# Kernel tuning notes

Hardware: AMD Instinct MI355X
Metric: run time of the kernel (lower is better)

Reference implementation:

```python
import jax, jax.numpy as jnp
import numpy as np

D_IN = 1024
D_OUT = 1024
NUM_HEADS = 16
HEAD_DIM = D_OUT // NUM_HEADS


def setup_inputs() -> dict:
    key = jax.random.key(0)
    ks = jax.random.split(key, 6)
    s = 0.02
    return {
        "x": jax.random.normal(ks[0], (4, 2048, D_IN), dtype=jnp.float32),
        "Wq": jax.random.normal(ks[1], (D_IN, D_OUT), dtype=jnp.float32) * s,
        "Wk": jax.random.normal(ks[2], (D_IN, D_OUT), dtype=jnp.float32) * s,
        "Wv": jax.random.normal(ks[3], (D_IN, D_OUT), dtype=jnp.float32) * s,
        "Wo": jax.random.normal(ks[4], (D_OUT, D_OUT), dtype=jnp.float32) * s,
        "bo": jax.random.normal(ks[5], (D_OUT,), dtype=jnp.float32) * s,
    }


def reference(x, Wq, Wk, Wv, Wo, bo):
    B, T, _ = x.shape
    H, Dh = NUM_HEADS, HEAD_DIM
    # projections -> [B, H, T, Dh]
    q = (x @ Wq).reshape(B, T, H, Dh).transpose(0, 2, 1, 3)
    k = (x @ Wk).reshape(B, T, H, Dh).transpose(0, 2, 1, 3)
    v = (x @ Wv).reshape(B, T, H, Dh).transpose(0, 2, 1, 3)
    # scores [B, H, T, T]
    scores = jnp.einsum('bhqd,bhkd->bhqk', q, k)
    causal = jnp.triu(jnp.ones((T, T), dtype=bool), k=1)
    scores = jnp.where(causal, -jnp.inf, scores)
    attn = jax.nn.softmax(scores / jnp.sqrt(jnp.float32(Dh)), axis=-1)
    # dropout=0.0 -> identity
    ctx = jnp.einsum('bhqk,bhkd->bhqd', attn, v)
    ctx = ctx.transpose(0, 2, 1, 3).reshape(B, T, H * Dh)
    return ctx @ Wo + bo
```

## Files before the change

kernel.cpp:

```cpp
#include <hip/hip_runtime.h>
#include <hip/hip_bf16.h>
#include <stdint.h>

#define TSEQ 2048
#define DMODEL 1024

typedef __attribute__((ext_vector_type(8))) short bf16x8;
typedef __attribute__((ext_vector_type(4))) float f32x4;
typedef __attribute__((ext_vector_type(16))) float f32x16;
typedef __attribute__((ext_vector_type(2))) int int2v;

union Frag { bf16x8 v; uint4 q; };

__device__ __forceinline__ uint16_t f2bfu(float f) {
  uint32_t u = __builtin_bit_cast(uint32_t, f);
  u += 0x7fffu + ((u >> 16) & 1u);
  return (uint16_t)(u >> 16);
}

__device__ __forceinline__ uint32_t pk2bf(float a, float b) {
  return ((uint32_t)f2bfu(b) << 16) | f2bfu(a);
}

__device__ __forceinline__ uint32_t cvtpk(float a, float b) {
  uint32_t r;
  asm("v_cvt_pk_bf16_f32 %0, %1, %2" : "=v"(r) : "v"(a), "v"(b));
  return r;
}

__device__ __forceinline__ void plane32swap(uint32_t& a, uint32_t& b) {
#if __has_builtin(__builtin_amdgcn_permlane32_swap)
  int2v r = __builtin_amdgcn_permlane32_swap((int)a, (int)b, false, false);
  a = (uint32_t)r[0];
  b = (uint32_t)r[1];
#else
  const uint32_t sa = (uint32_t)__shfl_xor((int)a, 32);
  const uint32_t sb = (uint32_t)__shfl_xor((int)b, 32);
  const bool hi = (threadIdx.x & 63) >= 32;
  const uint32_t na = hi ? sb : a;
  const uint32_t nb = hi ? b : sa;
  a = na;
  b = nb;
#endif
}

__device__ __forceinline__ float fexp2(float x) {
#if __has_builtin(__builtin_amdgcn_exp2f)
  return __builtin_amdgcn_exp2f(x);
#else
  return exp2f(x);
#endif
}

__device__ __forceinline__ void gload_lds16(const void* g, void* l) {
  __builtin_amdgcn_global_load_lds(
      (const __attribute__((address_space(1))) void*)g,
      (__attribute__((address_space(3))) void*)l, 16, 0, 0);
}


__global__ __launch_bounds__(256) void cvt_x_kernel(const float* __restrict__ x,
                                                    uint16_t* __restrict__ xb, int n4) {
  int i = blockIdx.x * 256 + threadIdx.x;
  if (i >= n4) return;
  float4 v = ((const float4*)x)[i];
  ushort4 o;
  o.x = f2bfu(v.x); o.y = f2bfu(v.y); o.z = f2bfu(v.z); o.w = f2bfu(v.w);
  ((ushort4*)xb)[i] = o;
}

__global__ __launch_bounds__(256) void cvt_w_kernel(const float* __restrict__ Wq,
    const float* __restrict__ Wk, const float* __restrict__ Wv, const float* __restrict__ Wo,
    uint16_t* __restrict__ Wqkvt, uint16_t* __restrict__ Wot) {
  const float* src = (blockIdx.z == 0) ? Wq : (blockIdx.z == 1) ? Wk
                   : (blockIdx.z == 2) ? Wv : Wo;
  uint16_t* dst = (blockIdx.z < 3) ? (Wqkvt + (size_t)blockIdx.z * DMODEL * DMODEL) : Wot;
  const float wscale = (blockIdx.z == 0) ? 0.125f * 1.4426950408889634f : 1.0f;
  __shared__ float tile[32][33];
  const int x0 = blockIdx.x * 32, y0 = blockIdx.y * 32;
  for (int ii = 0; ii < 4; ii++) {
    int i = threadIdx.y + ii * 8;
    tile[i][threadIdx.x] = src[(size_t)(y0 + i) * DMODEL + x0 + threadIdx.x];
  }
  __syncthreads();
  for (int ii = 0; ii < 4; ii++) {
    int i = threadIdx.y + ii * 8;
    dst[(size_t)(x0 + i) * DMODEL + y0 + threadIdx.x] = f2bfu(tile[threadIdx.x][i] * wscale);
  }
}

__device__ __forceinline__ void stage256(const char* Gb, int kb, char* ldsT, int tid) {
#pragma unroll
  for (int r = 0; r < 4; ++r) {
    const int u = tid + r * 512;
    const int row = u >> 3;
    const int sc = ((u & 7) * 16) ^ ((row & 7) << 4);
    gload_lds16(Gb + (size_t)row * 2048 + kb + sc, ldsT + u * 16);
  }
}


__device__ __forceinline__ void gemm256sq_core(const char* Ab, const char* Bb,
                                               char* lds,
                                               f32x4 (&acc)[8][4]) {
  const int tid = threadIdx.x;
  const int lane = tid & 63;
  const int w = tid >> 6;
  const int lr = lane & 15, lg = lane >> 4;
  const int wmb = (w >> 2) * 128;
  const int wnb = (w & 3) * 64;
  char* const A0 = lds;
  char* const A1 = lds + 32768;
  char* const B0 = lds + 65536;
  char* const B1 = lds + 98304;

#pragma unroll
  for (int i = 0; i < 8; i++)
#pragma unroll
    for (int j = 0; j < 4; j++) acc[i][j] = (f32x4){0.f, 0.f, 0.f, 0.f};

  stage256(Ab, 0, A0, tid);
  stage256(Bb, 0, B0, tid);
  for (int t = 0; t < 16; ++t) {
    const char* At = (t & 1) ? A1 : A0;
    const char* Bt = (t & 1) ? B1 : B0;
    char* nA = (t & 1) ? A0 : A1;
    char* nB = (t & 1) ? B0 : B1;
    if (t + 1 < 16) {
      stage256(Ab, (t + 1) * 128, nA, tid);
      asm volatile("s_waitcnt vmcnt(4)" ::: "memory");
    } else {
      asm volatile("s_waitcnt vmcnt(0)" ::: "memory");
    }
    __builtin_amdgcn_s_barrier();
    __builtin_amdgcn_sched_barrier(0);

    Frag bf0[4], bf1[4];
#pragma unroll
    for (int ni = 0; ni < 4; ni++) {
      const int row = wnb + ni * 16 + lr;
      const int swz = (row & 7) << 4;
      bf0[ni].q = *(const uint4*)(Bt + row * 128 + ((lg * 16) ^ swz));
      bf1[ni].q = *(const uint4*)(Bt + row * 128 + ((64 + lg * 16) ^ swz));
    }
#pragma unroll
    for (int ph = 0; ph < 4; ph++) {
      Frag a0[2], a1[2];
#pragma unroll
      for (int i = 0; i < 2; i++) {
        const int row = wmb + (2 * ph + i) * 16 + lr;
        const int swz = (row & 7) << 4;
        a0[i].q = *(const uint4*)(At + row * 128 + ((lg * 16) ^ swz));
        a1[i].q = *(const uint4*)(At + row * 128 + ((64 + lg * 16) ^ swz));
      }
      __builtin_amdgcn_s_setprio(1);
#pragma unroll
      for (int i = 0; i < 2; i++) {
        const int mi = 2 * ph + i;
#pragma unroll
        for (int ni = 0; ni < 4; ni++) {
          acc[mi][ni] = __builtin_amdgcn_mfma_f32_16x16x32_bf16(a0[i].v, bf0[ni].v,
                                                                acc[mi][ni], 0, 0, 0);
          acc[mi][ni] = __builtin_amdgcn_mfma_f32_16x16x32_bf16(a1[i].v, bf1[ni].v,
                                                                acc[mi][ni], 0, 0, 0);
        }
      }
      __builtin_amdgcn_s_setprio(0);
      if (ph == 0 && t + 1 < 16) stage256(Bb, (t + 1) * 128, nB, tid);
    }
    __builtin_amdgcn_s_barrier();
  }
}


__device__ __forceinline__ void g8_stage_p1(const char* Ab, int kb, char* ldsA, int tid) {
#pragma unroll
  for (int r = 0; r < 3; ++r) {
    const int u = tid + r * 512;
    const int row = u >> 3;
    const int sc = ((u & 7) * 16) ^ ((row & 7) << 4);
    gload_lds16(Ab + (size_t)row * 2048 + kb + sc, ldsA + u * 16);
  }
}

__device__ __forceinline__ void g8_stage_p2(const char* Ab, const char* Bb, int kb,
                                            char* ldsA, char* ldsB, int tid) {
  {
    const int u = tid + 3 * 512;
    const int row = u >> 3;
    const int sc = ((u & 7) * 16) ^ ((row & 7) << 4);
    gload_lds16(Ab + (size_t)row * 2048 + kb + sc, ldsA + u * 16);
  }
#pragma unroll
  for (int r = 0; r < 2; ++r) {
    const int u = tid + r * 512;
    const int row = u >> 3;
    const int sc = ((u & 7) * 16) ^ ((row & 7) << 4);
    gload_lds16(Bb + (size_t)row * 2048 + kb + sc, ldsB + u * 16);
  }
}

__device__ __forceinline__ void gemm256x128_core(const char* Ab, const char* Bb,
                                                 char* lds,
                                                 f32x4 (&acc)[4][4]) {
  const int tid = threadIdx.x;
  const int lane = tid & 63;
  const int w = tid >> 6;
  const int lr = lane & 15, lg = lane >> 4;
  const int wmb = (w >> 1) * 64;
  const int wnb = (w & 1) * 64;
  char* const A0 = lds;
  char* const A1 = lds + 32768;
  char* const B0 = lds + 65536;
  char* const B1 = lds + 81920;

#pragma unroll
  for (int i = 0; i < 4; i++)
#pragma unroll
    for (int j = 0; j < 4; j++) acc[i][j] = (f32x4){0.f, 0.f, 0.f, 0.f};

  g8_stage_p1(Ab, 0, A0, tid);
  g8_stage_p2(Ab, Bb, 0, A0, B0, tid);
  for (int t = 0; t < 16; ++t) {
    const char* At = (t & 1) ? A1 : A0;
    const char* Bt = (t & 1) ? B1 : B0;
    char* nA = (t & 1) ? A0 : A1;
    char* nB = (t & 1) ? B0 : B1;
    if (t + 1 < 16) {
      g8_stage_p1(Ab, (t + 1) * 128, nA, tid);
      asm volatile("s_waitcnt vmcnt(3)" ::: "memory");
    } else {
      asm volatile("s_waitcnt vmcnt(0)" ::: "memory");
    }
    __builtin_amdgcn_s_barrier();
    __builtin_amdgcn_sched_barrier(0);

    Frag bf0[4], bf1[4];
#pragma unroll
    for (int ni = 0; ni < 4; ni++) {
      const int row = wnb + ni * 16 + lr;
      const int swz = (row & 7) << 4;
      bf0[ni].q = *(const uint4*)(Bt + row * 128 + ((lg * 16) ^ swz));
      bf1[ni].q = *(const uint4*)(Bt + row * 128 + ((64 + lg * 16) ^ swz));
    }
    Frag pa0[2], pa1[2];
#pragma unroll
    for (int mi = 0; mi < 2; mi++) {
      const int row = wmb + mi * 16 + lr;
      const int swz = (row & 7) << 4;
      pa0[mi].q = *(const uint4*)(At + row * 128 + ((lg * 16) ^ swz));
      pa1[mi].q = *(const uint4*)(At + row * 128 + ((64 + lg * 16) ^ swz));
    }
    __builtin_amdgcn_s_setprio(1);
#pragma unroll
    for (int mi = 0; mi < 2; mi++)
#pragma unroll
      for (int ni = 0; ni < 4; ni++) {
        acc[mi][ni] = __builtin_amdgcn_mfma_f32_16x16x32_bf16(pa0[mi].v, bf0[ni].v,
                                                              acc[mi][ni], 0, 0, 0);
        acc[mi][ni] = __builtin_amdgcn_mfma_f32_16x16x32_bf16(pa1[mi].v, bf1[ni].v,
                                                              acc[mi][ni], 0, 0, 0);
      }
    __builtin_amdgcn_s_setprio(0);

    if (t + 1 < 16) g8_stage_p2(Ab, Bb, (t + 1) * 128, nA, nB, tid);
#pragma unroll
    for (int mi = 2; mi < 4; mi++) {
      const int row = wmb + mi * 16 + lr;
      const int swz = (row & 7) << 4;
      Frag qa0, qa1;
      qa0.q = *(const uint4*)(At + row * 128 + ((lg * 16) ^ swz));
      qa1.q = *(const uint4*)(At + row * 128 + ((64 + lg * 16) ^ swz));
      __builtin_amdgcn_s_setprio(1);
#pragma unroll
      for (int ni = 0; ni < 4; ni++) {
        acc[mi][ni] = __builtin_amdgcn_mfma_f32_16x16x32_bf16(qa0.v, bf0[ni].v,
                                                              acc[mi][ni], 0, 0, 0);
        acc[mi][ni] = __builtin_amdgcn_mfma_f32_16x16x32_bf16(qa1.v, bf1[ni].v,
                                                              acc[mi][ni], 0, 0, 0);
      }
      __builtin_amdgcn_s_setprio(0);
    }
    __builtin_amdgcn_s_barrier();
  }
}


__global__ __launch_bounds__(512, 2) void gemm_qkv_fused(const uint16_t* __restrict__ Xb,
    const uint16_t* __restrict__ Wt, uint16_t* __restrict__ Qo,
    uint16_t* __restrict__ Ko, uint16_t* __restrict__ Vt) {
  __shared__ __align__(16) char lds[131072];
  const int tid = threadIdx.x, w = tid >> 6, lane = tid & 63;
  const int lr = lane & 15, lg = lane >> 4;

  if (blockIdx.x < 256) {
    const int m0 = (blockIdx.x & 31) * 256;
    const int n0 = (blockIdx.x >> 5) * 256;
    f32x4 acc[8][4];
    gemm256sq_core((const char*)Xb + (size_t)m0 * 2048, (const char*)Wt + (size_t)n0 * 2048,
                   lds, acc);
    const int wmb = (w >> 2) * 128, wnb = (w & 3) * 64;
#pragma unroll
    for (int mi = 0; mi < 8; mi++)
#pragma unroll
      for (int ni = 0; ni < 4; ni++) {
        const int col = n0 + wnb + ni * 16 + lr;
        const int p = col >> 10, c = col & 1023, h = c >> 6, d = c & 63;
#pragma unroll
        for (int r = 0; r < 4; r++) {
          const int row = m0 + wmb + mi * 16 + 4 * lg + r;
          const int bb = row >> 11, t = row & 2047;
          const int bh = bb * 16 + h;
          const uint16_t val = f2bfu(acc[mi][ni][r]);
          if (p == 0) Qo[((size_t)bh * TSEQ + t) * 64 + d] = val;
          else        Ko[((size_t)bh * TSEQ + t) * 64 + d] = val;
        }
      }
  } else {
    const int vb = blockIdx.x - 256;
    const int m0 = (vb & 31) * 256;
    const int n0 = (vb >> 5) * 128;
    const uint16_t* Wtv = Wt + (size_t)2048 * 1024;
    f32x4 acc[4][4];
    gemm256x128_core((const char*)Xb + (size_t)m0 * 2048, (const char*)Wtv + (size_t)n0 * 2048,
                     lds, acc);
    const int wmb = (w >> 1) * 64;
    char* vr = lds + (w & 1) * 33792;
#pragma unroll
    for (int mi = 0; mi < 4; mi++)
#pragma unroll
      for (int ni = 0; ni < 4; ni++) {
        const int d = ni * 16 + lr;
        const int tl = wmb + mi * 16 + 4 * lg;
        uint2 pr;
        pr.x = cvtpk(acc[mi][ni][0], acc[mi][ni][1]);
        pr.y = cvtpk(acc[mi][ni][2], acc[mi][ni][3]);
        *(uint2*)(vr + d * 528 + tl * 2) = pr;
      }
    __syncthreads();
    const int bb = m0 >> 11, t0 = m0 & 2047;
    const int h0 = n0 >> 6;
#pragma unroll
    for (int j = 0; j < 8; j++) {
      const int linear = (tid + j * 512) * 16;
      const int rg = linear >> 15;
      const int rem = linear & 32767;
      const int d = rem >> 9;
      const int toff = rem & 511;
      const uint4 val = *(const uint4*)(lds + rg * 33792 + d * 528 + toff);
      const int bh = bb * 16 + h0 + rg;
      *(uint4*)((char*)Vt + ((size_t)(bh * 64 + d) * TSEQ + t0) * 2 + toff) = val;
    }
  }
}


__device__ __forceinline__ void stage_kv(const char* Kb, const char* Vb, int kv0,
                                         char* kdst, char* vdst, int tid) {
  const int w1024 = (tid >> 6) * 1024;
#pragma unroll
  for (int i = 0; i < 2; i++) {
    const int o = i * 4096 + tid * 16;
    const int row = o >> 7;
    const int scol = (o & 127) ^ ((row & 7) << 4);
    gload_lds16(Kb + (size_t)(kv0 + row) * 128 + scol, kdst + i * 4096 + w1024);
    gload_lds16(Vb + (size_t)row * 4096 + kv0 * 2 + scol, vdst + i * 4096 + w1024);
  }
}

__global__ __launch_bounds__(256, 4) void attn_kernel(const uint16_t* __restrict__ Qw,
    const uint16_t* __restrict__ Kw, const uint16_t* __restrict__ Vtw,
    uint16_t* __restrict__ Ctx) {
  const int bid = blockIdx.x;
  const int c = bid & 255;
  const int rd = bid >> 8;
  const int g = c >> 6;
  int qt;
  if (rd == 0)      qt = 15 - g;
  else if (rd == 1) qt = 8 + g;
  else if (rd == 2) qt = 7 - g;
  else              qt = g;
  const int bh = c & 63;
  const int tid = threadIdx.x;
  const int w = tid >> 6, lane = tid & 63;
  const int lq = lane & 31;
  const int hi = lane >> 5;
  const int wq0 = qt * 128 + w * 32;

  const char* Qb = (const char*)Qw + (size_t)bh * TSEQ * 128;
  const char* Kb = (const char*)Kw + (size_t)bh * TSEQ * 128;
  const char* Vb = (const char*)Vtw + (size_t)bh * 64 * 4096;

  __shared__ __align__(16) char kbuf[2][8192];
  __shared__ __align__(16) char vbuf[2][8192];

  Frag qa[4];
#pragma unroll
  for (int kc = 0; kc < 4; kc++)
    qa[kc].q = *(const uint4*)(Qb + (size_t)(wq0 + lq) * 128 + kc * 32 + hi * 16);

  f32x16 o0 = 0.f, o1 = 0.f;
  float mrun = -1e30f, lrun = 0.f;

  const int nt = 2 * qt + 2;
  stage_kv(Kb, Vb, 0, kbuf[0], vbuf[0], tid);
  int cur = 0;
  for (int t = 0; t < nt; ++t) {
    const int kv0 = t * 64;
    if (t + 1 < nt) {
      stage_kv(Kb, Vb, kv0 + 64, kbuf[cur ^ 1], vbuf[cur ^ 1], tid);
      asm volatile("s_waitcnt vmcnt(4)" ::: "memory");
    } else {
      asm volatile("s_waitcnt vmcnt(0)" ::: "memory");
    }
    __builtin_amdgcn_s_barrier();
    __builtin_amdgcn_sched_barrier(0);

    if (kv0 <= wq0 + 31) {
      const char* Kt = kbuf[cur];
      const char* Vt = vbuf[cur];
      f32x16 s[2];
#pragma unroll
      for (int kvh = 0; kvh < 2; kvh++) {
        f32x16 acc = 0.f;
#pragma unroll
        for (int kc = 0; kc < 4; kc++) {
          const int row = kvh * 32 + lq;
          Frag kf;
          kf.q = *(const uint4*)(Kt + row * 128 + ((kc * 32 + hi * 16) ^ ((row & 7) << 4)));
          acc = __builtin_amdgcn_mfma_f32_32x32x16_bf16(kf.v, qa[kc].v, acc, 0, 0, 0);
        }
        s[kvh] = acc;
      }
      if (kv0 + 63 > wq0) {
        const int q_abs = wq0 + lq;
#pragma unroll
        for (int kvh = 0; kvh < 2; kvh++)
#pragma unroll
          for (int r = 0; r < 16; r++) {
            const int kv_abs = kv0 + kvh * 32 + (r & 3) + 8 * (r >> 2) + 4 * hi;
            if (kv_abs > q_abs) s[kvh][r] = -1e30f;
          }
      }
      float t8[8];
#pragma unroll
      for (int i = 0; i < 8; i++)
        t8[i] = fmaxf(fmaxf(s[0][2 * i], s[0][2 * i + 1]),
                      fmaxf(s[1][2 * i], s[1][2 * i + 1]));
      float t4a = fmaxf(t8[0], t8[1]), t4b = fmaxf(t8[2], t8[3]);
      float t4c = fmaxf(t8[4], t8[5]), t4d = fmaxf(t8[6], t8[7]);
      float mt = fmaxf(fmaxf(t4a, t4b), fmaxf(t4c, t4d));
      mt = fmaxf(mt, __shfl_xor(mt, 32));
      if (!__all(mt - mrun <= 8.0f)) {
        const float mnew = fmaxf(mrun, mt);
        const float corr = fexp2(mrun - mnew);
        mrun = mnew;
        lrun *= corr;
        o0 *= corr;
        o1 *= corr;
      }
#pragma unroll
      for (int kvh = 0; kvh < 2; kvh++)
#pragma unroll
        for (int r = 0; r < 16; r++) s[kvh][r] = fexp2(s[kvh][r] - mrun);
      float ps = 0.f;
#pragma unroll
      for (int kvh = 0; kvh < 2; kvh++)
#pragma unroll
        for (int r = 0; r < 16; r++) ps += s[kvh][r];
      ps += __shfl_xor(ps, 32);
      lrun += ps;
      uint32_t pk[2][8];
#pragma unroll
      for (int kvh = 0; kvh < 2; kvh++)
#pragma unroll
        for (int j = 0; j < 8; j++)
          pk[kvh][j] = cvtpk(s[kvh][2 * j], s[kvh][2 * j + 1]);
#pragma unroll
      for (int c16 = 0; c16 < 4; c16++) {
        const int kvh = c16 >> 1, cl = c16 & 1;
        uint32_t x0 = pk[kvh][4 * cl + 0], y0 = pk[kvh][4 * cl + 2];
        uint32_t x1 = pk[kvh][4 * cl + 1], y1 = pk[kvh][4 * cl + 3];
        plane32swap(x0, y0);
        plane32swap(x1, y1);
        Frag pb;
        pb.q.x = x0;
        pb.q.y = x1;
        pb.q.z = y0;
        pb.q.w = y1;
#pragma unroll
        for (int dblk = 0; dblk < 2; dblk++) {
          const int row = dblk * 32 + lq;
          Frag vf;
          vf.q = *(const uint4*)(Vt + row * 128 + ((c16 * 32 + hi * 16) ^ ((row & 7) << 4)));
          if (dblk == 0)
            o0 = __builtin_amdgcn_mfma_f32_32x32x16_bf16(vf.v, pb.v, o0, 0, 0, 0);
          else
            o1 = __builtin_amdgcn_mfma_f32_32x32x16_bf16(vf.v, pb.v, o1, 0, 0, 0);
        }
      }
    }
    __builtin_amdgcn_s_barrier();
    cur ^= 1;
  }

  const int bb = bh >> 4, hh = bh & 15;
  const float inv = 1.0f / lrun;
  const int q_abs = wq0 + lq;
  uint16_t* crow = Ctx + ((size_t)bb * TSEQ + q_abs) * DMODEL + hh * 64;
#pragma unroll
  for (int dblk = 0; dblk < 2; dblk++)
#pragma unroll
    for (int g2 = 0; g2 < 4; g2++) {
      const float a0 = (dblk ? o1[4 * g2 + 0] : o0[4 * g2 + 0]) * inv;
      const float a1 = (dblk ? o1[4 * g2 + 1] : o0[4 * g2 + 1]) * inv;
      const float a2 = (dblk ? o1[4 * g2 + 2] : o0[4 * g2 + 2]) * inv;
      const float a3 = (dblk ? o1[4 * g2 + 3] : o0[4 * g2 + 3]) * inv;
      uint2 st;
      st.x = cvtpk(a0, a1);
      st.y = cvtpk(a2, a3);
      *(uint2*)(crow + dblk * 32 + 8 * g2 + 4 * hi) = st;
    }
}


__global__ __launch_bounds__(512, 2) void gemm_out_kernel(const uint16_t* __restrict__ Cb,
    const uint16_t* __restrict__ Wot, const float* __restrict__ bo,
    float* __restrict__ out) {
  __shared__ __align__(16) char lds[98304];
  const int m0 = (blockIdx.x & 31) * 256;
  const int n0 = (blockIdx.x >> 5) * 128;
  f32x4 acc[4][4];
  gemm256x128_core((const char*)Cb + (size_t)m0 * 2048, (const char*)Wot + (size_t)n0 * 2048,
                   lds, acc);

  const int tid = threadIdx.x, w = tid >> 6, lane = tid & 63;
  const int lr = lane & 15, lg = lane >> 4;
  const int wmb = (w >> 1) * 64, wnb = (w & 1) * 64;
#pragma unroll
  for (int mi = 0; mi < 4; mi++)
#pragma unroll
    for (int ni = 0; ni < 4; ni++) {
      const int col = n0 + wnb + ni * 16 + lr;
      const float bias = bo[col];
#pragma unroll
      for (int r = 0; r < 4; r++) {
        const int row = m0 + wmb + mi * 16 + 4 * lg + r;
        out[(size_t)row * DMODEL + col] = acc[mi][ni][r] + bias;
      }
    }
}


extern "C" void kernel_launch(void* const* d_in, const int* in_sizes, int n_in,
                              void* d_out, int out_size, void* d_ws, size_t ws_size,
                              hipStream_t stream) {
  const float* x  = (const float*)d_in[0];
  const float* Wq = (const float*)d_in[1];
  const float* Wk = (const float*)d_in[2];
  const float* Wv = (const float*)d_in[3];
  const float* Wo = (const float*)d_in[4];
  const float* bo = (const float*)d_in[5];
  float* out = (float*)d_out;

  char* ws = (char*)d_ws;
  uint16_t* Xb    = (uint16_t*)(ws);
  uint16_t* Ctx   = (uint16_t*)(ws);
  uint16_t* Wqkvt = (uint16_t*)(ws + (16u << 20));
  uint16_t* Wot   = (uint16_t*)(ws + (22u << 20));
  uint16_t* Qw    = (uint16_t*)(ws + (24u << 20));
  uint16_t* Kw    = (uint16_t*)(ws + (40u << 20));
  uint16_t* Vtw   = (uint16_t*)(ws + (56u << 20));
  (void)ws_size; (void)in_sizes; (void)n_in; (void)out_size;

  cvt_x_kernel<<<8192, 256, 0, stream>>>(x, Xb, 2097152);
  cvt_w_kernel<<<dim3(32, 32, 4), dim3(32, 8), 0, stream>>>(Wq, Wk, Wv, Wo, Wqkvt, Wot);
  gemm_qkv_fused<<<512, 512, 0, stream>>>(Xb, Wqkvt, Qw, Kw, Vtw);
  attn_kernel<<<1024, 256, 0, stream>>>(Qw, Kw, Vtw, Ctx);
  gemm_out_kernel<<<256, 512, 0, stream>>>(Ctx, Wot, bo, out);
}
```

Measured before the change: 157.4 us.

## Merge conversion kernels and restructure GEMM core into quadrant-phased staging

```diff
diff --git a/kernel.cpp b/kernel.cpp
--- a/kernel.cpp
+++ b/kernel.cpp
@@ -16,10 +16,6 @@
   uint32_t u = __builtin_bit_cast(uint32_t, f);
   u += 0x7fffu + ((u >> 16) & 1u);
   return (uint16_t)(u >> 16);
-}
-
-__device__ __forceinline__ uint32_t pk2bf(float a, float b) {
-  return ((uint32_t)f2bfu(b) << 16) | f2bfu(a);
 }
 
 __device__ __forceinline__ uint32_t cvtpk(float a, float b) {
@@ -59,39 +55,53 @@
 }
 
 
-__global__ __launch_bounds__(256) void cvt_x_kernel(const float* __restrict__ x,
-                                                    uint16_t* __restrict__ xb, int n4) {
-  int i = blockIdx.x * 256 + threadIdx.x;
-  if (i >= n4) return;
-  float4 v = ((const float4*)x)[i];
-  ushort4 o;
-  o.x = f2bfu(v.x); o.y = f2bfu(v.y); o.z = f2bfu(v.z); o.w = f2bfu(v.w);
-  ((ushort4*)xb)[i] = o;
-}
-
-__global__ __launch_bounds__(256) void cvt_w_kernel(const float* __restrict__ Wq,
-    const float* __restrict__ Wk, const float* __restrict__ Wv, const float* __restrict__ Wo,
-    uint16_t* __restrict__ Wqkvt, uint16_t* __restrict__ Wot) {
-  const float* src = (blockIdx.z == 0) ? Wq : (blockIdx.z == 1) ? Wk
-                   : (blockIdx.z == 2) ? Wv : Wo;
-  uint16_t* dst = (blockIdx.z < 3) ? (Wqkvt + (size_t)blockIdx.z * DMODEL * DMODEL) : Wot;
-  const float wscale = (blockIdx.z == 0) ? 0.125f * 1.4426950408889634f : 1.0f;
+__global__ __launch_bounds__(256) void cvt_all_kernel(const float* __restrict__ x,
+    const float* __restrict__ Wq, const float* __restrict__ Wk,
+    const float* __restrict__ Wv, const float* __restrict__ Wo,
+    uint16_t* __restrict__ xb, uint16_t* __restrict__ Wqkvt, uint16_t* __restrict__ Wot) {
+  const int bid = blockIdx.x;
+  const int tid = threadIdx.x;
+  if (bid < 8192) {
+    const int i = bid * 256 + tid;
+    float4 v = ((const float4*)x)[i];
+    ushort4 o;
+    o.x = f2bfu(v.x); o.y = f2bfu(v.y); o.z = f2bfu(v.z); o.w = f2bfu(v.w);
+    ((ushort4*)xb)[i] = o;
+    return;
+  }
+  const int r = bid - 8192;
+  const int wz = r >> 10;
+  const int by = (r & 1023) >> 5;
+  const int bx = r & 31;
+  const float* src = (wz == 0) ? Wq : (wz == 1) ? Wk : (wz == 2) ? Wv : Wo;
+  uint16_t* dst = (wz < 3) ? (Wqkvt + (size_t)wz * DMODEL * DMODEL) : Wot;
+  const float wscale = (wz == 0) ? 0.125f * 1.4426950408889634f : 1.0f;
   __shared__ float tile[32][33];
-  const int x0 = blockIdx.x * 32, y0 = blockIdx.y * 32;
+  const int x0 = bx * 32, y0 = by * 32;
+  const int tx = tid & 31, ty = tid >> 5;
   for (int ii = 0; ii < 4; ii++) {
-    int i = threadIdx.y + ii * 8;
-    tile[i][threadIdx.x] = src[(size_t)(y0 + i) * DMODEL + x0 + threadIdx.x];
+    int i = ty + ii * 8;
+    tile[i][tx] = src[(size_t)(y0 + i) * DMODEL + x0 + tx];
   }
   __syncthreads();
   for (int ii = 0; ii < 4; ii++) {
-    int i = threadIdx.y + ii * 8;
-    dst[(size_t)(x0 + i) * DMODEL + y0 + threadIdx.x] = f2bfu(tile[threadIdx.x][i] * wscale);
+    int i = ty + ii * 8;
+    dst[(size_t)(x0 + i) * DMODEL + y0 + tx] = f2bfu(tile[tx][i] * wscale);
   }
 }
 
 __device__ __forceinline__ void stage256(const char* Gb, int kb, char* ldsT, int tid) {
 #pragma unroll
   for (int r = 0; r < 4; ++r) {
+    const int u = tid + r * 512;
+    const int row = u >> 3;
+    const int sc = ((u & 7) * 16) ^ ((row & 7) << 4);
+    gload_lds16(Gb + (size_t)row * 2048 + kb + sc, ldsT + u * 16);
+  }
+}
+__device__ __forceinline__ void stage_half256(const char* Gb, int kb, char* ldsT, int tid) {
+#pragma unroll
+  for (int r = 0; r < 2; ++r) {
     const int u = tid + r * 512;
     const int row = u >> 3;
     const int sc = ((u & 7) * 16) ^ ((row & 7) << 4);
@@ -119,55 +129,103 @@
 #pragma unroll
     for (int j = 0; j < 4; j++) acc[i][j] = (f32x4){0.f, 0.f, 0.f, 0.f};
 
-  stage256(Ab, 0, A0, tid);
-  stage256(Bb, 0, B0, tid);
+  stage_half256(Ab, 0, A0, tid);
+  stage_half256(Ab + (size_t)128 * 2048, 0, A0 + 16384, tid);
+  stage_half256(Bb, 0, B0, tid);
+  stage_half256(Bb + (size_t)128 * 2048, 0, B0 + 16384, tid);
+
   for (int t = 0; t < 16; ++t) {
     const char* At = (t & 1) ? A1 : A0;
     const char* Bt = (t & 1) ? B1 : B0;
     char* nA = (t & 1) ? A0 : A1;
     char* nB = (t & 1) ? B0 : B1;
+    const int nkb = (t + 1) * 128;
+
     if (t + 1 < 16) {
-      stage256(Ab, (t + 1) * 128, nA, tid);
-      asm volatile("s_waitcnt vmcnt(4)" ::: "memory");
+      stage_half256(Ab, nkb, nA, tid);
+      asm volatile("s_waitcnt vmcnt(2)" ::: "memory");
     } else {
       asm volatile("s_waitcnt vmcnt(0)" ::: "memory");
     }
     __builtin_amdgcn_s_barrier();
     __builtin_amdgcn_sched_barrier(0);
 
-    Frag bf0[4], bf1[4];
-#pragma unroll
-    for (int ni = 0; ni < 4; ni++) {
-      const int row = wnb + ni * 16 + lr;
+    Frag a0[4], a1[4];
+    Frag b00[2], b01[2];
+    Frag b10[2], b11[2];
+#pragma unroll
+    for (int i = 0; i < 4; i++) {
+      const int row = wmb + i * 16 + lr;
       const int swz = (row & 7) << 4;
-      bf0[ni].q = *(const uint4*)(Bt + row * 128 + ((lg * 16) ^ swz));
-      bf1[ni].q = *(const uint4*)(Bt + row * 128 + ((64 + lg * 16) ^ swz));
-    }
-#pragma unroll
-    for (int ph = 0; ph < 4; ph++) {
-      Frag a0[2], a1[2];
-#pragma unroll
-      for (int i = 0; i < 2; i++) {
-        const int row = wmb + (2 * ph + i) * 16 + lr;
-        const int swz = (row & 7) << 4;
-        a0[i].q = *(const uint4*)(At + row * 128 + ((lg * 16) ^ swz));
-        a1[i].q = *(const uint4*)(At + row * 128 + ((64 + lg * 16) ^ swz));
-      }
-      __builtin_amdgcn_s_setprio(1);
-#pragma unroll
-      for (int i = 0; i < 2; i++) {
-        const int mi = 2 * ph + i;
-#pragma unroll
-        for (int ni = 0; ni < 4; ni++) {
-          acc[mi][ni] = __builtin_amdgcn_mfma_f32_16x16x32_bf16(a0[i].v, bf0[ni].v,
-                                                                acc[mi][ni], 0, 0, 0);
-          acc[mi][ni] = __builtin_amdgcn_mfma_f32_16x16x32_bf16(a1[i].v, bf1[ni].v,
-                                                                acc[mi][ni], 0, 0, 0);
-        }
-      }
-      __builtin_amdgcn_s_setprio(0);
-      if (ph == 0 && t + 1 < 16) stage256(Bb, (t + 1) * 128, nB, tid);
-    }
+      a0[i].q = *(const uint4*)(At + row * 128 + ((lg * 16) ^ swz));
+      a1[i].q = *(const uint4*)(At + row * 128 + ((64 + lg * 16) ^ swz));
+    }
+#pragma unroll
+    for (int i = 0; i < 2; i++) {
+      const int row = wnb + i * 16 + lr;
+      const int swz = (row & 7) << 4;
+      b00[i].q = *(const uint4*)(Bt + row * 128 + ((lg * 16) ^ swz));
+      b01[i].q = *(const uint4*)(Bt + row * 128 + ((64 + lg * 16) ^ swz));
+    }
+    if (t + 1 < 16) stage_half256(Ab + (size_t)128 * 2048, nkb, nA + 16384, tid);
+    __builtin_amdgcn_s_setprio(1);
+#pragma unroll
+    for (int i = 0; i < 4; i++)
+#pragma unroll
+      for (int j = 0; j < 2; j++) {
+        acc[i][j] = __builtin_amdgcn_mfma_f32_16x16x32_bf16(a0[i].v, b00[j].v, acc[i][j], 0, 0, 0);
+        acc[i][j] = __builtin_amdgcn_mfma_f32_16x16x32_bf16(a1[i].v, b01[j].v, acc[i][j], 0, 0, 0);
+      }
+    __builtin_amdgcn_s_setprio(0);
+    __builtin_amdgcn_s_barrier();
+
+#pragma unroll
+    for (int i = 0; i < 2; i++) {
+      const int row = wnb + (2 + i) * 16 + lr;
+      const int swz = (row & 7) << 4;
+      b10[i].q = *(const uint4*)(Bt + row * 128 + ((lg * 16) ^ swz));
+      b11[i].q = *(const uint4*)(Bt + row * 128 + ((64 + lg * 16) ^ swz));
+    }
+    if (t + 1 < 16) stage_half256(Bb, nkb, nB, tid);
+    __builtin_amdgcn_s_setprio(1);
+#pragma unroll
+    for (int i = 0; i < 4; i++)
+#pragma unroll
+      for (int j = 0; j < 2; j++) {
+        acc[i][2 + j] = __builtin_amdgcn_mfma_f32_16x16x32_bf16(a0[i].v, b10[j].v, acc[i][2 + j], 0, 0, 0);
+        acc[i][2 + j] = __builtin_amdgcn_mfma_f32_16x16x32_bf16(a1[i].v, b11[j].v, acc[i][2 + j], 0, 0, 0);
+      }
+    __builtin_amdgcn_s_setprio(0);
+    __builtin_amdgcn_s_barrier();
+
+#pragma unroll
+    for (int i = 0; i < 4; i++) {
+      const int row = wmb + (4 + i) * 16 + lr;
+      const int swz = (row & 7) << 4;
+      a0[i].q = *(const uint4*)(At + row * 128 + ((lg * 16) ^ swz));
+      a1[i].q = *(const uint4*)(At + row * 128 + ((64 + lg * 16) ^ swz));
+    }
+    if (t + 1 < 16) stage_half256(Bb + (size_t)128 * 2048, nkb, nB + 16384, tid);
+    __builtin_amdgcn_s_setprio(1);
+#pragma unroll
+    for (int i = 0; i < 4; i++)
+#pragma unroll
+      for (int j = 0; j < 2; j++) {
+        acc[4 + i][2 + j] = __builtin_amdgcn_mfma_f32_16x16x32_bf16(a0[i].v, b10[j].v, acc[4 + i][2 + j], 0, 0, 0);
+        acc[4 + i][2 + j] = __builtin_amdgcn_mfma_f32_16x16x32_bf16(a1[i].v, b11[j].v, acc[4 + i][2 + j], 0, 0, 0);
+      }
+    __builtin_amdgcn_s_setprio(0);
+    __builtin_amdgcn_s_barrier();
+
+    __builtin_amdgcn_s_setprio(1);
+#pragma unroll
+    for (int i = 0; i < 4; i++)
+#pragma unroll
+      for (int j = 0; j < 2; j++) {
+        acc[4 + i][j] = __builtin_amdgcn_mfma_f32_16x16x32_bf16(a0[i].v, b00[j].v, acc[4 + i][j], 0, 0, 0);
+        acc[4 + i][j] = __builtin_amdgcn_mfma_f32_16x16x32_bf16(a1[i].v, b01[j].v, acc[4 + i][j], 0, 0, 0);
+      }
+    __builtin_amdgcn_s_setprio(0);
     __builtin_amdgcn_s_barrier();
   }
 }
@@ -573,8 +631,7 @@
   uint16_t* Vtw   = (uint16_t*)(ws + (56u << 20));
   (void)ws_size; (void)in_sizes; (void)n_in; (void)out_size;
 
-  cvt_x_kernel<<<8192, 256, 0, stream>>>(x, Xb, 2097152);
-  cvt_w_kernel<<<dim3(32, 32, 4), dim3(32, 8), 0, stream>>>(Wq, Wk, Wv, Wo, Wqkvt, Wot);
+  cvt_all_kernel<<<12288, 256, 0, stream>>>(x, Wq, Wk, Wv, Wo, Xb, Wqkvt, Wot);
   gemm_qkv_fused<<<512, 512, 0, stream>>>(Xb, Wqkvt, Qw, Kw, Vtw);
   attn_kernel<<<1024, 256, 0, stream>>>(Qw, Kw, Vtw, Ctx);
   gemm_out_kernel<<<256, 512, 0, stream>>>(Ctx, Wot, bo, out);
```

New measurement: 151.2 us. -3.9%, faster.
